# Kernel optimization log

Hardware: AMD Instinct MI355X
Metric: run time of the kernel (lower is better)

Reference implementation:

```python
import jax, jax.numpy as jnp
import numpy as np

N_NODES = 50000
N_EDGES = 800000


def setup_inputs() -> dict:
    key = jax.random.key(0)
    ks = jax.random.split(key, 8)
    x = jax.random.normal(ks[0], (N_NODES, 256), dtype=jnp.float32)
    edge_index = jax.random.randint(ks[1], (2, N_EDGES), 0, N_NODES, dtype=jnp.int64)
    edge_weight = jax.random.uniform(ks[2], (N_EDGES,), dtype=jnp.float32)
    # Glorot-style weights for the 3 GCNConv layers: 256->128->64->32
    def glorot(k, fan_in, fan_out):
        s = jnp.sqrt(6.0 / (fan_in + fan_out))
        return jax.random.uniform(k, (fan_in, fan_out), dtype=jnp.float32, minval=-s, maxval=s)
    return {
        "x": x,
        "edge_index": edge_index,
        "edge_weight": edge_weight,
        "W1": glorot(ks[3], 256, 128), "b1": jnp.zeros((128,), jnp.float32),
        "W2": glorot(ks[4], 128, 64),  "b2": jnp.zeros((64,), jnp.float32),
        "W3": glorot(ks[5], 64, 32),   "b3": jnp.zeros((32,), jnp.float32),
    }


def _gcn_forward(x, row, col, ew, params):
    """Stacked GCNConv+ReLU (PyG semantics: add self loops, symmetric norm)."""
    n = x.shape[0]
    loop = jnp.arange(n, dtype=row.dtype)
    row_f = jnp.concatenate([row, loop])            # [E+N] sources
    col_f = jnp.concatenate([col, loop])            # [E+N] targets
    ew_f = jnp.concatenate([ew, jnp.ones((n,), ew.dtype)])
    deg = jax.ops.segment_sum(ew_f, col_f, num_segments=n)
    dinv = jnp.where(deg > 0, jax.lax.rsqrt(deg), 0.0)
    norm = dinv[row_f] * ew_f * dinv[col_f]         # [E+N]
    for W, b in params:
        h = x @ W                                   # [N, d_out] linear first (PyG order)
        msg = h[row_f] * norm[:, None]              # [E+N, d_out] gather + scale
        agg = jax.ops.segment_sum(msg, col_f, num_segments=n)  # scatter-add
        x = jax.nn.relu(agg + b)                    # fused bias + ReLU
    return x


def reference(x, edge_index, edge_weight, W1, b1, W2, b2, W3, b3):
    row, col = edge_index[0], edge_index[1]
    params = [(W1, b1), (W2, b2), (W3, b3)]
    return _gcn_forward(x, row, col, edge_weight, params)
```

## Files before the change

kernel.cpp:

```cpp
#include <hip/hip_runtime.h>
#include <hip/hip_fp16.h>


#define D0 256
#define D1 128
#define D2 64
#define D3 32

#define FIX_SCALE 16777216.0f
#define FIX_INV   (1.0f / 16777216.0f)

typedef _Float16 half8 __attribute__((ext_vector_type(8)));
typedef float floatx4 __attribute__((ext_vector_type(4)));

template <typename SRC>
__device__ __forceinline__ half8 loadA(const SRC* __restrict__ p) {
    if constexpr (sizeof(SRC) == 4) {
        float4 f0 = *(const float4*)p;
        float4 f1 = *(const float4*)(p + 4);
        half8 v;
        v[0] = (_Float16)f0.x; v[1] = (_Float16)f0.y;
        v[2] = (_Float16)f0.z; v[3] = (_Float16)f0.w;
        v[4] = (_Float16)f1.x; v[5] = (_Float16)f1.y;
        v[6] = (_Float16)f1.z; v[7] = (_Float16)f1.w;
        return v;
    } else {
        return *(const half8*)p;
    }
}

template <int K, int BN, typename SRC>
__device__ __forceinline__ void gemm_work(const SRC* __restrict__ X,
                                          const float* __restrict__ W,
                                          _Float16* __restrict__ H, int N,
                                          int w, int totalWaves) {
    constexpr int NC = K / 32;
    constexpr int CG = BN / 32;
    const int lane = threadIdx.x & 63;
    const int quad = lane >> 4;
    const int m = lane & 15;
    const int cg = w & (CG - 1);
    const int nslab = N >> 4;
    const int stride = totalWaves / CG;
    int slab = w / CG;
    if (slab >= nslab) return;
    const int n0 = cg * 32;

    half8 b0[NC], b1[NC];
#pragma unroll
    for (int c = 0; c < NC; ++c) {
#pragma unroll
        for (int j = 0; j < 8; ++j) {
            int k = c * 32 + quad * 8 + j;
            b0[c][j] = (_Float16)W[(size_t)k * BN + n0 + m];
            b1[c][j] = (_Float16)W[(size_t)k * BN + n0 + 16 + m];
        }
    }

    half8 a[NC];
#pragma unroll
    for (int c = 0; c < NC; ++c)
        a[c] = loadA(&X[(size_t)(slab * 16 + m) * K + c * 32 + quad * 8]);

    while (true) {
        const int next = slab + stride;
        half8 an[NC];
        if (next < nslab) {
#pragma unroll
            for (int c = 0; c < NC; ++c)
                an[c] = loadA(&X[(size_t)(next * 16 + m) * K + c * 32 + quad * 8]);
        }

        floatx4 acc0 = (floatx4){0.f, 0.f, 0.f, 0.f};
        floatx4 acc1 = (floatx4){0.f, 0.f, 0.f, 0.f};
#pragma unroll
        for (int c = 0; c < NC; ++c) {
            acc0 = __builtin_amdgcn_mfma_f32_16x16x32_f16(a[c], b0[c], acc0, 0, 0, 0);
            acc1 = __builtin_amdgcn_mfma_f32_16x16x32_f16(a[c], b1[c], acc1, 0, 0, 0);
        }

        const int r0 = slab * 16 + quad * 4;
#pragma unroll
        for (int r = 0; r < 4; ++r) {
            H[(size_t)(r0 + r) * BN + n0 + m]      = (_Float16)acc0[r];
            H[(size_t)(r0 + r) * BN + n0 + 16 + m] = (_Float16)acc1[r];
        }

        if (next >= nslab) break;
        slab = next;
#pragma unroll
        for (int c = 0; c < NC; ++c) a[c] = an[c];
    }
}

__global__ __launch_bounds__(256) void hist_gemm1_kernel(
        const float* __restrict__ x, const float* __restrict__ W1,
        _Float16* __restrict__ h1, int N,
        const int* __restrict__ ei, const float* __restrict__ ew,
        unsigned long long* __restrict__ pk, int* __restrict__ rank, int E,
        int gB) {
    const int b = blockIdx.x;
    if (b < gB) {
        gemm_work<D0, D1, float>(x, W1, h1, N, b * 4 + (threadIdx.x >> 6), gB * 4);
    } else {
        int e = (b - gB) * 256 + threadIdx.x;
        if (e < E) {
            int c = ei[E + e];
            unsigned int wfix = (unsigned int)(ew[e] * FIX_SCALE + 0.5f);
            unsigned long long old =
                atomicAdd(&pk[c], (1ULL << 32) | (unsigned long long)wfix);
            rank[e] = (int)(old >> 32);
        }
    }
}

template <int K, int BN, typename SRC>
__global__ __launch_bounds__(256) void mfma_gemm(const SRC* __restrict__ X,
                                                 const float* __restrict__ W,
                                                 _Float16* __restrict__ H, int N) {
    gemm_work<K, BN, SRC>(X, W, H, N, blockIdx.x * 4 + (threadIdx.x >> 6), gridDim.x * 4);
}

__global__ __launch_bounds__(256) void scan_reduce(const unsigned long long* __restrict__ pk,
                                                   float* __restrict__ dinv,
                                                   int* __restrict__ cnt,
                                                   int* __restrict__ blockSum, int N) {
    __shared__ int s[256];
    const int t = threadIdx.x;
    const int i = blockIdx.x * 256 + t;
    int v = 0;
    if (i < N) {
        unsigned long long p = pk[i];
        float d = (float)(unsigned int)(p & 0xffffffffULL) * FIX_INV + 1.0f;
        dinv[i] = rsqrtf(d);
        v = (int)(p >> 32);
        cnt[i] = v;
    }
    s[t] = v;
    __syncthreads();
#pragma unroll
    for (int off = 128; off > 0; off >>= 1) {
        if (t < off) s[t] += s[t + off];
        __syncthreads();
    }
    if (t == 0) blockSum[blockIdx.x] = s[0];
}

__global__ __launch_bounds__(256) void scan_apply(const int* __restrict__ cnt,
                                                  const int* __restrict__ blockSum,
                                                  int* __restrict__ row_ptr, int N, int B) {
    __shared__ int bs[256];
    __shared__ int s[256];
    const int t = threadIdx.x;
    bs[t] = (t < B) ? blockSum[t] : 0;
    __syncthreads();
#pragma unroll
    for (int off = 1; off < 256; off <<= 1) {
        int u = (t >= off) ? bs[t - off] : 0;
        __syncthreads();
        bs[t] += u;
        __syncthreads();
    }
    const int myOff = (blockIdx.x > 0) ? bs[blockIdx.x - 1] : 0;
    const int i = blockIdx.x * 256 + t;
    const int v = (i < N) ? cnt[i] : 0;
    s[t] = v;
    __syncthreads();
#pragma unroll
    for (int off = 1; off < 256; off <<= 1) {
        int u = (t >= off) ? s[t - off] : 0;
        __syncthreads();
        s[t] += u;
        __syncthreads();
    }
    if (i < N) row_ptr[i] = s[t] - v + myOff;
    if (blockIdx.x == 0 && t == 0) row_ptr[N] = bs[B - 1];
}

__global__ void fill_kernel(const int* __restrict__ ei, const float* __restrict__ ew,
                            const float* __restrict__ dinv,
                            const int* __restrict__ row_ptr, const int* __restrict__ rank,
                            int2* __restrict__ pairs, int E) {
    int e = blockIdx.x * blockDim.x + threadIdx.x;
    if (e < E) {
        int r = ei[e];
        int c = ei[E + e];
        float w = dinv[r] * ew[e] * dinv[c];
        pairs[row_ptr[c] + rank[e]] = make_int2(r, __float_as_int(w));
    }
}

template <int D, typename OUT>
__global__ __launch_bounds__(256) void agg_kernel(const _Float16* __restrict__ H,
                                                  const int* __restrict__ row_ptr,
                                                  const int2* __restrict__ pairs,
                                                  const float* __restrict__ dinv,
                                                  const float* __restrict__ bias,
                                                  OUT* __restrict__ out, int N) {
    constexpr int TPN = D / 8;
    constexpr int NPB = 256 / TPN;
    const int tid = threadIdx.x;
    const int g = tid / TPN;
    const int lane = tid % TPN;
    const int node = blockIdx.x * NPB + g;
    if (node >= N) return;

    const int beg = row_ptr[node];
    const int end = row_ptr[node + 1];
    float acc[8];
#pragma unroll
    for (int j = 0; j < 8; ++j) acc[j] = 0.0f;

    if (end > beg) {
        const int last = end - 1;
        int2 p0 = pairs[beg];
        int2 p1 = pairs[min(beg + 1, last)];
        int2 p2 = pairs[min(beg + 2, last)];
        half8 u0 = *(const half8*)&H[(size_t)p0.x * D + lane * 8];
        half8 u1 = *(const half8*)&H[(size_t)p1.x * D + lane * 8];
        for (int k = beg; k < end; ++k) {
            int2 p3 = pairs[min(k + 3, last)];
            half8 u2 = *(const half8*)&H[(size_t)p2.x * D + lane * 8];
            float w = __int_as_float(p0.y);
#pragma unroll
            for (int j = 0; j < 8; ++j) acc[j] = fmaf(w, (float)u0[j], acc[j]);
            p0 = p1; p1 = p2; p2 = p3;
            u0 = u1; u1 = u2;
        }
    }
    float di = dinv[node];
    float d2 = di * di;
    {
        half8 u = *(const half8*)&H[(size_t)node * D + lane * 8];
#pragma unroll
        for (int j = 0; j < 8; ++j) acc[j] = fmaf(d2, (float)u[j], acc[j]);
    }
    float b[8];
    *(float4*)&b[0] = *(const float4*)&bias[lane * 8];
    *(float4*)&b[4] = *(const float4*)&bias[lane * 8 + 4];
#pragma unroll
    for (int j = 0; j < 8; ++j) acc[j] = fmaxf(acc[j] + b[j], 0.f);

    if constexpr (sizeof(OUT) == 2) {
        half8 o;
#pragma unroll
        for (int j = 0; j < 8; ++j) o[j] = (_Float16)acc[j];
        *(half8*)&out[(size_t)node * D + lane * 8] = o;
    } else {
        float* dst = (float*)&out[(size_t)node * D + lane * 8];
        *(float4*)&dst[0] = make_float4(acc[0], acc[1], acc[2], acc[3]);
        *(float4*)&dst[4] = make_float4(acc[4], acc[5], acc[6], acc[7]);
    }
}

extern "C" void kernel_launch(void* const* d_in, const int* in_sizes, int n_in,
                              void* d_out, int out_size, void* d_ws, size_t ws_size,
                              hipStream_t stream) {
    const float* x   = (const float*)d_in[0];
    const int* ei    = (const int*)d_in[1];
    const float* ew  = (const float*)d_in[2];
    const float* W1  = (const float*)d_in[3];
    const float* b1  = (const float*)d_in[4];
    const float* W2  = (const float*)d_in[5];
    const float* b2  = (const float*)d_in[6];
    const float* W3  = (const float*)d_in[7];
    const float* b3  = (const float*)d_in[8];
    float* out = (float*)d_out;

    const int N = in_sizes[0] / D0;
    const int E = in_sizes[2];
    (void)n_in; (void)out_size; (void)ws_size;

    char* ws = (char*)d_ws;
    size_t off = 0;
    auto carve = [&](size_t bytes) -> void* {
        void* p = (void*)(ws + off);
        off += (bytes + 255) & ~(size_t)255;
        return p;
    };
    unsigned long long* pk = (unsigned long long*)carve((size_t)N * 8);
    float* dinv    = (float*)carve((size_t)N * 4);
    int*   cnt     = (int*)carve((size_t)N * 4);
    int*   row_ptr = (int*)carve((size_t)(N + 1) * 4);
    int*   rank    = (int*)carve((size_t)E * 4);
    int*   bsum    = (int*)carve(256 * 4);
    int2*  pairs   = (int2*)carve((size_t)E * 8);
    _Float16* bufH = (_Float16*)carve((size_t)N * D1 * 2);
    _Float16* bufO = (_Float16*)carve((size_t)N * D1 * 2);

    _Float16* h1   = bufH;
    _Float16* out1 = bufO;
    _Float16* h2   = bufH;
    _Float16* out2 = bufO;
    _Float16* h3   = bufH;

    const int eb = (E + 255) / 256;
    const int scanB = (N + 255) / 256;
    const int gB = 768;

    hipMemsetAsync(pk, 0, (size_t)N * 8, stream);
    hist_gemm1_kernel<<<gB + eb, 256, 0, stream>>>(
        x, W1, h1, N, ei, ew, pk, rank, E, gB);

    scan_reduce<<<scanB, 256, 0, stream>>>(pk, dinv, cnt, bsum, N);
    scan_apply<<<scanB, 256, 0, stream>>>(cnt, bsum, row_ptr, N, scanB);
    fill_kernel<<<eb, 256, 0, stream>>>(ei, ew, dinv, row_ptr, rank, pairs, E);

    agg_kernel<D1, _Float16><<<(N + 15) / 16, 256, 0, stream>>>(h1, row_ptr, pairs, dinv, b1, out1, N);

    mfma_gemm<D1, D2, _Float16><<<gB, 256, 0, stream>>>(out1, W2, h2, N);
    agg_kernel<D2, _Float16><<<(N + 31) / 32, 256, 0, stream>>>(h2, row_ptr, pairs, dinv, b2, out2, N);

    mfma_gemm<D2, D3, _Float16><<<gB, 256, 0, stream>>>(out2, W3, h3, N);
    agg_kernel<D3, float><<<(N + 63) / 64, 256, 0, stream>>>(h3, row_ptr, pairs, dinv, b3, out, N);
}
```

Baseline: 260.9 us.

## Use atomic work-stealing for edge histogram and deepen aggregation prefetch

The fused GEMM1 and histogram kernel now hands out edge work dynamically. Every wavefront, the GEMM wavefronts included once they finish, takes 64-edge chunks from a global counter, which the memset zeroes together with the degree array. This is meant to balance GEMM and histogram work across the grid instead of using one block per 256 edges. Separately, the aggregation kernel's software pipeline is deepened by one stage, so three feature-row loads are in flight instead of two, at the cost of extra registers.

```diff
diff --git a/kernel.cpp b/kernel.cpp
--- a/kernel.cpp
+++ b/kernel.cpp
@@ -98,17 +98,24 @@
         _Float16* __restrict__ h1, int N,
         const int* __restrict__ ei, const float* __restrict__ ew,
         unsigned long long* __restrict__ pk, int* __restrict__ rank, int E,
-        int gB) {
+        int* __restrict__ ctr, int gB) {
     const int b = blockIdx.x;
-    if (b < gB) {
+    if (b < gB)
         gemm_work<D0, D1, float>(x, W1, h1, N, b * 4 + (threadIdx.x >> 6), gB * 4);
-    } else {
-        int e = (b - gB) * 256 + threadIdx.x;
+
+    const int lane = threadIdx.x & 63;
+    const int nChunks = (E + 63) >> 6;
+    for (;;) {
+        int c = 0;
+        if (lane == 0) c = atomicAdd(ctr, 1);
+        c = __shfl(c, 0);
+        if (c >= nChunks) break;
+        int e = c * 64 + lane;
         if (e < E) {
-            int c = ei[E + e];
+            int col = ei[E + e];
             unsigned int wfix = (unsigned int)(ew[e] * FIX_SCALE + 0.5f);
             unsigned long long old =
-                atomicAdd(&pk[c], (1ULL << 32) | (unsigned long long)wfix);
+                atomicAdd(&pk[col], (1ULL << 32) | (unsigned long long)wfix);
             rank[e] = (int)(old >> 32);
         }
     }
@@ -216,16 +223,18 @@
         int2 p0 = pairs[beg];
         int2 p1 = pairs[min(beg + 1, last)];
         int2 p2 = pairs[min(beg + 2, last)];
+        int2 p3 = pairs[min(beg + 3, last)];
         half8 u0 = *(const half8*)&H[(size_t)p0.x * D + lane * 8];
         half8 u1 = *(const half8*)&H[(size_t)p1.x * D + lane * 8];
+        half8 u2 = *(const half8*)&H[(size_t)p2.x * D + lane * 8];
         for (int k = beg; k < end; ++k) {
-            int2 p3 = pairs[min(k + 3, last)];
-            half8 u2 = *(const half8*)&H[(size_t)p2.x * D + lane * 8];
+            int2 p4 = pairs[min(k + 4, last)];
+            half8 u3 = *(const half8*)&H[(size_t)p3.x * D + lane * 8];
             float w = __int_as_float(p0.y);
 #pragma unroll
             for (int j = 0; j < 8; ++j) acc[j] = fmaf(w, (float)u0[j], acc[j]);
-            p0 = p1; p1 = p2; p2 = p3;
-            u0 = u1; u1 = u2;
+            p0 = p1; p1 = p2; p2 = p3; p3 = p4;
+            u0 = u1; u1 = u2; u2 = u3;
         }
     }
     float di = dinv[node];
@@ -279,6 +288,7 @@
         return p;
     };
     unsigned long long* pk = (unsigned long long*)carve((size_t)N * 8);
+    int*   ctr     = (int*)carve(256);
     float* dinv    = (float*)carve((size_t)N * 4);
     int*   cnt     = (int*)carve((size_t)N * 4);
     int*   row_ptr = (int*)carve((size_t)(N + 1) * 4);
@@ -297,10 +307,12 @@
     const int eb = (E + 255) / 256;
     const int scanB = (N + 255) / 256;
     const int gB = 768;
-
-    hipMemsetAsync(pk, 0, (size_t)N * 8, stream);
-    hist_gemm1_kernel<<<gB + eb, 256, 0, stream>>>(
-        x, W1, h1, N, ei, ew, pk, rank, E, gB);
+    const int histB = 1024;
+
+    size_t pkBytes = (((size_t)N * 8 + 255) & ~(size_t)255) + 256;
+    hipMemsetAsync(pk, 0, pkBytes, stream);
+    hist_gemm1_kernel<<<gB + histB, 256, 0, stream>>>(
+        x, W1, h1, N, ei, ew, pk, rank, E, ctr, gB);
 
     scan_reduce<<<scanB, 256, 0, stream>>>(pk, dinv, cnt, bsum, N);
     scan_apply<<<scanB, 256, 0, stream>>>(cnt, bsum, row_ptr, N, scanB);
```

New measurement: 459.1 us. 1.76x slower.
